# Performance work log

Measured on AMD Instinct MI355X. Metric: run time of the kernel, lower is better.

Reference implementation:

```python
import jax, jax.numpy as jnp
import numpy as np

SR = 22050
FLOOR = 60.0
BPO = 12

def _interp_linear(p, T):
    # torch F.interpolate(mode='linear', align_corners=False)
    S = p.shape[0]
    x = np.clip((np.arange(T, dtype=np.float64) + 0.5) * (S / T) - 0.5, 0.0, S - 1)
    i0 = np.floor(x).astype(np.int64)
    i1 = np.minimum(i0 + 1, S - 1)
    f = (x - i0).astype(np.float32)
    return p[i0] * (1.0 - f) + p[i1] * f

def _hann(n):
    # torch.hann_window(n, periodic=True)
    if n <= 0:
        return np.zeros((0,), np.float32)
    return (0.5 - 0.5 * np.cos(2.0 * np.pi * np.arange(n) / n)).astype(np.float32)

def _find_voiced(f0, i):
    sub = f0[i:]
    if sub.size == 0:
        return None
    flag = (sub > 0.0).astype(np.int64)
    flag[0] = 0
    if not flag.any():
        return None
    rel = int(flag.argmax())
    after = flag[rel:]
    z = np.nonzero(after == 0)[0]
    run = int(z[0]) if z.size else int(after.size)
    return i + rel, i + rel + run

def _l2n(v):
    # F.normalize(dim=-1), eps=1e-12
    return v / np.maximum(np.linalg.norm(v, axis=-1, keepdims=True), 1e-12)

def _find_peak(signal, f0, i, right_dir):
    w = int(SR / max(float(f0[i]), FLOOR))
    s = max(i - w // 2, 0)
    if right_dir:
        cand_l, cand_r = int(i + 0.3 * w), int(i + 0.75 * w)
    else:
        cand_l, cand_r = max(int(i - 1.75 * w), 0), max(int(i - 1.3 * w), 0)
    if cand_l == cand_r or len(signal) - cand_l < w:
        return w, -1.0, i, 0.0
    seg = np.lib.stride_tricks.sliding_window_view(signal[cand_l:cand_r + w], w)
    corr = _l2n(seg) @ _l2n(signal[s:s + w])
    r = int(corr.argmax())
    return w, float(corr[r]), i + (r + cand_l) - s, float(np.abs(seg[r]).max())

def _find_allpeaks(signal, f0):
    gp = float(np.abs(signal).max())
    added_right, i, peaks = -1e308, 0, []
    while True:
        voiced = _find_voiced(f0, i)
        if voiced is None:
            break
        left, right = voiced
        middle = (left + right) // 2
        w = int(SR / float(f0[middle]))
        s = max(middle - w // 2, 0)
        seg = signal[s:s + w]
        mn, imn = float(seg.min()), int(seg.argmin())
        mx, imx = float(seg.max()), int(seg.argmax())
        i = middle if mn == mx else s + (imn if abs(mn) > abs(mx) else imx)
        backup = i
        while True:
            w, corr, i, peak = _find_peak(signal, f0, i, False)
            if corr == -1.0:
                i -= w
            if i < left:
                if corr > 0.7 and peak > 0.023333 * gp and i - added_right > 0.8 * w:
                    peaks.append(i)
                break
            if corr > 0.3 and (peak == 0.0 or peak > 0.01 * gp):
                if i - added_right > 0.8 * w:
                    peaks.append(i)
        i = backup
        while True:
            w, corr, i, peak = _find_peak(signal, f0, i, True)
            if corr == -1.0:
                i += w
            if i >= right:
                if corr > 0.7 and peak > 0.023333 * gp:
                    peaks.append(i)
                    added_right = i
                break
            if corr > 0.3 and (peak == 0.0 or peak > 0.01 * gp):
                peaks.append(i)
                added_right = i
        i = right
    if not peaks:
        return None
    return np.clip(np.array(sorted(peaks), dtype=np.int64), 0, len(signal) - 1)

def _psola_plan(signal, pitch, peaks):
    # Returns list of (dst_idx, src_idx, window) overlap-add ops plus tail index.
    T = len(signal)
    idx = np.arange(T)
    max_w = 1.25 * SR / float(pitch[pitch > 0].min())
    ops, i = [], 0
    while i < T:
        voiced = _find_voiced(pitch, i)
        if voiced is None:
            break
        left_v, right_v = voiced
        if i < left_v:
            ops.append((idx[i:left_v], idx[i:left_v], _hann(left_v - i)))
        while left_v < right_v:
            p = int(np.abs(peaks - left_v).argmin())
            period = int(SR / max(float(pitch[left_v]), FLOOR))
            left_w = right_w = period // 2
            if p > 0 and peaks[p] - peaks[p - 1] <= max_w:
                left_w = min(int(peaks[p] - peaks[p - 1]), left_w)
            if p < len(peaks) - 1 and peaks[p + 1] - peaks[p] <= max_w:
                right_w = min(int(peaks[p + 1] - peaks[p]), right_w)
            left_i = max(int(peaks[p]) - left_w, 0)
            right_i = int(peaks[p]) + right_w
            ival = (right_i - left_i) // 2
            if ival <= 0:  # safety guard; unreachable for speech-range pitch
                break
            win = _hann(ival * 2)
            seglen = min(len(idx[left_v - ival:left_v + ival]), len(idx[left_i:left_i + ival * 2]))
            dst = idx[left_v - ival:left_v - ival + seglen]
            src = idx[left_i:left_i + seglen]
            L = min(len(dst), len(src), seglen)
            ops.append((dst[:L], src[:L], win[:L]))
            left_v += ival * 2
        i = right_v
    return ops, i

def _pitch_shift_plan(snd, pitch, steps, pitch_range):
    if not (pitch > 1e-05).any():
        return None
    f0 = _interp_linear(pitch, len(snd))
    peaks = _find_allpeaks(snd, f0)
    if peaks is None:
        return None
    v = np.sort(pitch[pitch > 0.0])
    median = float(v[(len(v) - 1) // 2])  # torch lower median
    factor = 2.0 ** (steps / BPO)
    f0, median = f0 * factor, median * factor
    f0 = np.where(f0 > 0.0, median + (f0 - median) * pitch_range, 0.0).astype(np.float32)
    return _psola_plan(snd, f0, peaks)

def setup_inputs():
    key = jax.random.key(0)
    T, S = 661500, 3000
    t = np.arange(S)
    base = (170.0 + 40.0 * np.sin(2.0 * np.pi * t / 400.0)).astype(np.float32)
    voiced = (t % 75) >= 15  # alternating unvoiced/voiced runs
    pitch = np.where(voiced, base, 0.0).astype(np.float32)
    f0 = _interp_linear(pitch, T)
    phase = 2.0 * np.pi * np.cumsum(f0.astype(np.float64)) / SR
    noise = np.asarray(jax.random.normal(key, (T,)), np.float32)
    snd = np.where(f0 > 0.0, 0.55 * np.sin(phase) + 0.25 * np.sin(2 * phase) + 0.1 * np.sin(3 * phase), 0.0)
    snd = np.clip(snd + 0.02 * noise, -1.0, 1.0).astype(np.float32)
    return {"snd": jnp.asarray(snd), "pitch": jnp.asarray(pitch), "steps": 3, "pitch_range": jnp.float32(1.0)}

def reference(snd, pitch, steps, pitch_range):
    snd_np = np.asarray(snd, np.float32)
    pitch_np = np.asarray(pitch, np.float32)
    plan = _pitch_shift_plan(snd_np, pitch_np, int(steps), float(pitch_range))
    if plan is None:
        return jnp.asarray(snd_np)
    ops, tail = plan
    out = np.zeros_like(snd_np)
    for dst, src, win in ops:
        out[dst] += win * snd_np[src]
    out[tail:] = snd_np[tail:]
    return jnp.asarray(out)
```

## Files before the change

kernel.cpp:

```cpp
#include <hip/hip_runtime.h>
#include <cfloat>
#include <climits>
#include <math.h>

#define SRATE 22050.0
#define WMAX 512
#define RCAP 128
#define LCR 256
#define RCR 512
#define SCAP 16384
#define OPR 256
#define MSL 3072
#define NTW 256
#define NTM 1024
#define PCAP 8192
#define FCAP 16384
#define PSTG 4096
#define SNDW 15872
#define RPW 136


__global__ __launch_bounds__(256) void kstats(const float* __restrict__ pitch, int S, unsigned* scal) {
  __shared__ float sp[MSL];
  __shared__ int sc[256];
  __shared__ int sa[256];
  __shared__ unsigned hist[256];
  __shared__ unsigned sprefix, smask;
  __shared__ int srank;
  int tid = threadIdx.x;
  if (tid < 64) scal[tid] = (tid == 1) ? 0x7f800000u : 0u;
  bool lds = (S <= MSL);
  int c = 0, a = 0;
  for (int j = tid; j < S; j += 256) {
    float v = pitch[j];
    if (lds) sp[j] = v;
    if (v > 0.0f) c++;
    if (v > 1e-05f) a = 1;
  }
  sc[tid] = c; sa[tid] = a; __syncthreads();
  for (int st = 128; st; st >>= 1) {
    if (tid < st) { sc[tid] += sc[tid + st]; sa[tid] |= sa[tid + st]; }
    __syncthreads();
  }
  int n = sc[0];
  if (tid == 0) { scal[15] = (unsigned)n; scal[3] = (unsigned)sa[0]; }
  if (n == 0) return;
  if (tid == 0) { sprefix = 0u; smask = 0u; srank = (n - 1) >> 1; }
  __syncthreads();
  for (int shift = 24; shift >= 0; shift -= 8) {
    hist[tid] = 0u;
    __syncthreads();
    unsigned pfx = sprefix, msk = smask;
    for (int q = tid; q < S; q += 256) {
      float v = lds ? sp[q] : pitch[q];
      if (v > 0.0f) {
        unsigned u = __float_as_uint(v);
        if ((u & msk) == pfx) atomicAdd(&hist[(u >> shift) & 255u], 1u);
      }
    }
    __syncthreads();
    if (tid == 0) {
      int r = srank;
      unsigned b = 0;
      for (;;) { unsigned cc = hist[b]; if (r < (int)cc) break; r -= (int)cc; b++; }
      srank = r;
      sprefix = pfx | (b << shift);
      smask = msk | (0xFFu << shift);
    }
    __syncthreads();
  }
  if (tid == 0) scal[2] = sprefix;
}

__device__ __forceinline__ float interp1(const float* __restrict__ pitch, int S, double r, int t) {
  double x = ((double)t + 0.5) * r - 0.5;
  if (x < 0.0) x = 0.0;
  double sm1 = (double)(S - 1);
  if (x > sm1) x = sm1;
  double fl = floor(x);
  int i0 = (int)fl;
  int i1 = i0 + 1; if (i1 > S - 1) i1 = S - 1;
  float f = (float)(x - fl);
  return __fadd_rn(__fmul_rn(pitch[i0], __fsub_rn(1.0f, f)), __fmul_rn(pitch[i1], f));
}

__global__ __launch_bounds__(256) void kprep(const float* __restrict__ pitch, int S, int T,
                                             const float* __restrict__ snd, unsigned* scal,
                                             const int* __restrict__ steps_p, const float* __restrict__ pr_p,
                                             float* __restrict__ f0, float* __restrict__ f0s,
                                             int* __restrict__ pd, int* __restrict__ w0,
                                             int* s0l, int* e0l, int* s1l, int* e1l) {
  __shared__ float smax[256];
  __shared__ unsigned smin[256];
  float med = __uint_as_float(scal[2]);
  double factor = exp2((double)steps_p[0] / 12.0);
  float fac32 = (float)factor;
  float m32 = (float)((double)med * factor);
  float pr32 = pr_p[0];
  double r = (double)S / (double)T;
  float amax = 0.0f;
  unsigned lmin = 0x7f800000u;
  int stride = gridDim.x * blockDim.x;
  for (int t = blockIdx.x * blockDim.x + threadIdx.x; t < T; t += stride) {
    float v = interp1(pitch, S, r, t);
    f0[t] = v;
    float v1 = __fmul_rn(v, fac32);
    float vs = 0.0f;
    if (v1 > 0.0f) vs = __fadd_rn(m32, __fmul_rn(__fsub_rn(v1, m32), pr32));
    f0s[t] = vs;
    { double fd = (double)vs; if (fd < 60.0) fd = 60.0; pd[t] = (int)(SRATE / fd); }
    { double fi = (double)v; if (fi < 60.0) fi = 60.0;
      int ww = (int)(SRATE / fi); if (ww < 1) ww = 1; if (ww > WMAX - 1) ww = WMAX - 1;
      w0[t] = ww; }
    if (vs > 0.0f) { unsigned b = __float_as_uint(vs); if (b < lmin) lmin = b; }
    float a = fabsf(snd[t]); if (a > amax) amax = a;
    bool pv = false, pv1 = false;
    if (t > 0) {
      float pvv = interp1(pitch, S, r, t - 1);
      pv = pvv > 0.0f;
      float pm1 = __fmul_rn(pvv, fac32);
      float pvs = 0.0f;
      if (pm1 > 0.0f) pvs = __fadd_rn(m32, __fmul_rn(__fsub_rn(pm1, m32), pr32));
      pv1 = pvs > 0.0f;
    }
    bool cv = v > 0.0f, cv1 = vs > 0.0f;
    if (cv && (t == 0 || !pv))  { unsigned k = atomicAdd(scal + 8, 1u);  if (k < RCAP) s0l[k] = t; }
    if (!cv && t > 0 && pv)     { unsigned k = atomicAdd(scal + 9, 1u);  if (k < RCAP) e0l[k] = t; }
    if (cv1 && (t == 0 || !pv1)){ unsigned k = atomicAdd(scal + 10, 1u); if (k < RCAP) s1l[k] = t; }
    if (!cv1 && t > 0 && pv1)   { unsigned k = atomicAdd(scal + 11, 1u); if (k < RCAP) e1l[k] = t; }
  }
  smax[threadIdx.x] = amax; smin[threadIdx.x] = lmin; __syncthreads();
  for (int st = 128; st; st >>= 1) {
    if (threadIdx.x < st) {
      float o = smax[threadIdx.x + st]; if (o > smax[threadIdx.x]) smax[threadIdx.x] = o;
      unsigned u = smin[threadIdx.x + st]; if (u < smin[threadIdx.x]) smin[threadIdx.x] = u;
    }
    __syncthreads();
  }
  if (threadIdx.x == 0) {
    atomicMax(scal + 0, __float_as_uint(smax[0]));
    atomicMin(scal + 1, smin[0]);
  }
}

__device__ void ranksort(int* a, int n, int tid, int* tmp) {
  int v = 0, rk = 0;
  if (tid < n) {
    v = a[tid];
    for (int q = 0; q < n; q++) if (a[q] < v) rk++;
  }
  __syncthreads();
  if (tid < n) tmp[rk] = v;
  __syncthreads();
  if (tid < n) a[tid] = tmp[tid];
  __syncthreads();
}

__device__ int pair_regions_lds(float f1, int T, int* sl, int ns, int* el, int ne, int* L, int* R) {
  int b = 0;
  if (ns > 0 && sl[0] == 0) {
    if (T > 1 && f1 > 0.0f) sl[0] = 1;
    else b = 1;
  }
  int m = 0, j = 0;
  for (int k = b; k < ns; k++) {
    int Lv = sl[k];
    while (j < ne && el[j] <= Lv) j++;
    int Rv = (j < ne) ? el[j] : T;
    if (m < RCAP) { L[m] = Lv; R[m] = Rv; m++; }
  }
  return m;
}

__global__ __launch_bounds__(128) void kregsort2(const float* __restrict__ f0, const float* __restrict__ f0s,
                                                 int T, unsigned* scal,
                                                 const int* __restrict__ s0l, const int* __restrict__ e0l,
                                                 const int* __restrict__ s1l, const int* __restrict__ e1l,
                                                 int* r0L, int* r0R, int* r1L, int* r1R) {
  __shared__ int A[RCAP], B[RCAP], C[RCAP], D[RCAP];
  __shared__ int tmp[RCAP];
  __shared__ int LA[RCAP], RA[RCAP];
  int tid = threadIdx.x;
  int ns0 = min((int)scal[8], RCAP), ne0 = min((int)scal[9], RCAP);
  int ns1 = min((int)scal[10], RCAP), ne1 = min((int)scal[11], RCAP);
  if (tid < ns0) A[tid] = s0l[tid];
  if (tid < ne0) B[tid] = e0l[tid];
  if (tid < ns1) C[tid] = s1l[tid];
  if (tid < ne1) D[tid] = e1l[tid];
  __syncthreads();
  ranksort(A, ns0, tid, tmp);
  ranksort(B, ne0, tid, tmp);
  ranksort(C, ns1, tid, tmp);
  ranksort(D, ne1, tid, tmp);
  float f0_1 = (T > 1) ? f0[1] : 0.0f;
  float f0s_1 = (T > 1) ? f0s[1] : 0.0f;
  __shared__ int m0s, m1s;
  if (tid == 0) {
    m0s = pair_regions_lds(f0_1, T, A, ns0, B, ne0, LA, RA);
  }
  __syncthreads();
  if (tid < m0s) { r0L[tid] = LA[tid]; r0R[tid] = RA[tid]; }
  __syncthreads();
  if (tid == 0) {
    m1s = pair_regions_lds(f0s_1, T, C, ns1, D, ne1, LA, RA);
  }
  __syncthreads();
  if (tid < m1s) { r1L[tid] = LA[tid]; r1R[tid] = RA[tid]; }
  if (tid == 0) { scal[12] = (unsigned)m0s; scal[13] = (unsigned)m1s; }
}

struct FPRes { int w; int i; float corr; float peak; };
struct FPG { int w, s, cl, nw, rlen; bool ok; };

__device__ __forceinline__ FPG fp_geom(int T, int i, int w, bool right_dir) {
  FPG g;
  int s = i - w / 2; if (s < 0) s = 0;
  int cl, cr;
  if (right_dir) {
    cl = (int)((double)i + 0.3 * (double)w);
    cr = (int)((double)i + 0.75 * (double)w);
  } else {
    double al = (double)i - 1.75 * (double)w;
    double bl = (double)i - 1.3 * (double)w;
    cl = (int)al; if (cl < 0) cl = 0;
    cr = (int)bl; if (cr < 0) cr = 0;
  }
  g.w = w; g.s = s; g.cl = cl;
  g.ok = !(cl == cr || T - cl < w);
  int nw = (((cr + w) < T ? (cr + w) : T)) - cl - w + 1;
  if (nw < 1) nw = 1;
  g.nw = nw;
  int rlen = T - s; if (rlen > w) rlen = w;
  g.rlen = rlen;
  return g;
}

template <bool L>
__device__ __forceinline__ FPRes fp_impl(const float* __restrict__ snd, const float* lsnd, int wb0,
                                         FPG g, int i, int tid,
                                         float (*refp)[RPW], double* sdd, float* swf, int* swi, float* swp) {
  FPRes res;
  int w = g.w, s = g.s, cl = g.cl, nw = g.nw, rlen = g.rlen;
  res.w = w;
  int lane = tid & 63, wv = tid >> 6;
  double part = 0.0;
  for (int k = tid; k < w; k += NTW) {
    float v = (k < rlen) ? (L ? lsnd[s + k - wb0] : snd[s + k]) : 0.0f;
    refp[k & 3][k >> 2] = v;
    part += (double)v * (double)v;
  }
  for (int off = 32; off; off >>= 1) part += __shfl_xor(part, off, 64);
  if (lane == 0) sdd[wv] = part;
  __syncthreads();
  double refden = sqrt(sdd[0] + sdd[1] + sdd[2] + sdd[3]);
  if (refden < 1e-12) refden = 1e-12;
  int gg = tid >> 2, sub = tid & 3;
  float bestv = -FLT_MAX; int bestr = INT_MAX; float bestp = 0.0f;
  for (int base = 0; base < nw; base += 64) {
    int r = base + gg;
    if (r < nw) {
      const float* seg = (L ? (lsnd + (cl - wb0)) : (snd + cl)) + r;
      const float* rrow = refp[sub];
      double d0 = 0.0, d1 = 0.0, n0 = 0.0, n1 = 0.0;
      float pkc = 0.0f;
      int k = sub, j = 0;
      for (; k + 12 < w; k += 16, j += 4) {
        float4 rv = *reinterpret_cast<const float4*>(rrow + j);
        float a0f = seg[k], a1f = seg[k + 4];
        pkc = fmaxf(pkc, fabsf(a0f));
        pkc = fmaxf(pkc, fabsf(a1f));
        double a0 = (double)a0f, a1 = (double)a1f;
        d0 += a0 * (double)rv.x; n0 += a0 * a0;
        d1 += a1 * (double)rv.y; n1 += a1 * a1;
        float a2f = seg[k + 8], a3f = seg[k + 12];
        pkc = fmaxf(pkc, fabsf(a2f));
        pkc = fmaxf(pkc, fabsf(a3f));
        double a2 = (double)a2f, a3 = (double)a3f;
        d0 += a2 * (double)rv.z; n0 += a2 * a2;
        d1 += a3 * (double)rv.w; n1 += a3 * a3;
      }
      for (; k + 4 < w; k += 8) {
        float a0f = seg[k], a1f = seg[k + 4];
        pkc = fmaxf(pkc, fabsf(a0f));
        pkc = fmaxf(pkc, fabsf(a1f));
        double a0 = (double)a0f, b0 = (double)refp[k & 3][k >> 2];
        double a1 = (double)a1f, b1 = (double)refp[(k + 4) & 3][(k + 4) >> 2];
        d0 += a0 * b0; n0 += a0 * a0;
        d1 += a1 * b1; n1 += a1 * a1;
      }
      for (; k < w; k += 4) {
        float af = seg[k];
        pkc = fmaxf(pkc, fabsf(af));
        double a = (double)af; d0 += a * (double)refp[k & 3][k >> 2]; n0 += a * a;
      }
      double dot = d0 + d1, nr2 = n0 + n1;
      dot += __shfl_xor(dot, 1, 64); nr2 += __shfl_xor(nr2, 1, 64);
      pkc = fmaxf(pkc, __shfl_xor(pkc, 1, 64));
      dot += __shfl_xor(dot, 2, 64); nr2 += __shfl_xor(nr2, 2, 64);
      pkc = fmaxf(pkc, __shfl_xor(pkc, 2, 64));
      if (sub == 0) {
        double den = sqrt(nr2); if (den < 1e-12) den = 1e-12;
        float c = (float)(dot / (den * refden));
        if (c > bestv) { bestv = c; bestr = r; bestp = pkc; }
      }
    }
  }
  for (int off = 32; off >= 4; off >>= 1) {
    float ov = __shfl_xor(bestv, off, 64);
    int orr = __shfl_xor(bestr, off, 64);
    float op = __shfl_xor(bestp, off, 64);
    if (ov > bestv || (ov == bestv && orr < bestr)) { bestv = ov; bestr = orr; bestp = op; }
  }
  if (lane == 0) { swf[wv] = bestv; swi[wv] = bestr; swp[wv] = bestp; }
  __syncthreads();
  float bv = swf[0]; int br = swi[0]; float bp = swp[0];
  for (int q = 1; q < 4; q++) {
    float ov = swf[q]; int orr = swi[q]; float op = swp[q];
    if (ov > bv || (ov == bv && orr < br)) { bv = ov; br = orr; bp = op; }
  }
  res.corr = bv;
  res.i = i + (br + cl) - s;
  res.peak = bp;
  return res;
}

__device__ __forceinline__ FPRes find_peak_block(const float* __restrict__ snd,
                                                 const float* lsnd, int wb0, int wb1, bool useW,
                                                 int T, int i, int wcur, bool right_dir, int tid,
                                                 float (*refp)[RPW], double* sdd,
                                                 float* swf, int* swi, float* swp) {
  FPG g = fp_geom(T, i, wcur, right_dir);
  if (!g.ok) { FPRes r; r.w = g.w; r.corr = -1.0f; r.i = i; r.peak = 0.0f; return r; }
  int lo_a = g.s < g.cl ? g.s : g.cl;
  int hi1 = g.s + g.w, hi2 = g.cl + g.nw + g.w;
  int hi_a = hi1 > hi2 ? hi1 : hi2;
  bool inW = useW && lo_a >= wb0 && hi_a <= wb1;
  if (inW) return fp_impl<true>(snd, lsnd, wb0, g, i, tid, refp, sdd, swf, swi, swp);
  return fp_impl<false>(snd, lsnd, wb0, g, i, tid, refp, sdd, swf, swi, swp);
}

__global__ __launch_bounds__(NTW) void kwalk(const float* __restrict__ snd,
                                             const float* __restrict__ pitch, int S,
                                             const int* __restrict__ w0,
                                             int T, const unsigned* scal,
                                             const int* __restrict__ r0L, const int* __restrict__ r0R,
                                             int2* __restrict__ lcand, int* __restrict__ lcnt,
                                             int* __restrict__ rpk, int* __restrict__ rcnt) {
  __shared__ float lsnd[SNDW];
  __shared__ short swtab[SNDW];
  __shared__ __align__(16) float refp[4][RPW];
  __shared__ double sdd[4];
  __shared__ float swf[8];
  __shared__ int swi[8];
  __shared__ float swp[4];
  __shared__ float spitch[PSTG];
  int tid = threadIdx.x;
  int lane = tid & 63, wv = tid >> 6;
  if (scal[3] == 0u) return;
  bool useL = (S <= PSTG);
  if (useL) { for (int k = tid; k < S; k += NTW) spitch[k] = pitch[k]; }
  __syncthreads();
  double rr = (double)S / (double)T;
  int nreg = (int)scal[12];
  float gp = __uint_as_float(scal[0]);
  for (int wid = blockIdx.x; wid < 2 * nreg; wid += gridDim.x) {
    int r = wid >> 1;
    bool rightdir = (wid & 1) != 0;
    int left = r0L[r], right = r0R[r];
    int middle = (left + right) >> 1;
    int wb0 = left - 1024; if (wb0 < 0) wb0 = 0;
    int wb1 = right + 1024; if (wb1 > T) wb1 = T;
    bool useW = (wb1 - wb0) <= SNDW;
    __syncthreads();
    if (useW) {
      for (int k = tid; k < wb1 - wb0; k += NTW) {
        lsnd[k] = snd[wb0 + k];
        swtab[k] = (short)w0[wb0 + k];
      }
    }
    __syncthreads();
    double fm = useL ? (double)interp1(spitch, S, rr, middle) : (double)interp1(pitch, S, rr, middle);
    double wd = SRATE / fm;
    long long wcap = 2LL * (long long)T;
    int w = (wd >= (double)wcap) ? (int)wcap : (int)wd;
    if (w < 1) w = 1;
    int s0 = middle - w / 2; if (s0 < 0) s0 = 0;
    int wlen = w; if (wlen > T - s0) wlen = T - s0;
    float lmn = FLT_MAX; int lmni = INT_MAX;
    float lmx = -FLT_MAX; int lmxi = INT_MAX;
    for (int k = tid; k < wlen; k += NTW) {
      int idx = s0 + k;
      float v = (useW && idx >= wb0 && idx < wb1) ? lsnd[idx - wb0] : snd[idx];
      if (v < lmn) { lmn = v; lmni = k; }
      if (v > lmx) { lmx = v; lmxi = k; }
    }
    for (int off = 32; off; off >>= 1) {
      float ov = __shfl_xor(lmn, off, 64); int oi = __shfl_xor(lmni, off, 64);
      if (ov < lmn || (ov == lmn && oi < lmni)) { lmn = ov; lmni = oi; }
      float ov2 = __shfl_xor(lmx, off, 64); int oi2 = __shfl_xor(lmxi, off, 64);
      if (ov2 > lmx || (ov2 == lmx && oi2 < lmxi)) { lmx = ov2; lmxi = oi2; }
    }
    if (lane == 0) { swf[wv] = lmn; swi[wv] = lmni; swf[4 + wv] = lmx; swi[4 + wv] = lmxi; }
    __syncthreads();
    float mn = swf[0]; int imn = swi[0];
    float mx = swf[4]; int imx = swi[4];
    for (int q = 1; q < 4; q++) {
      float ov = swf[q]; int oi = swi[q];
      if (ov < mn || (ov == mn && oi < imn)) { mn = ov; imn = oi; }
      float ov2 = swf[4 + q]; int oi2 = swi[4 + q];
      if (ov2 > mx || (ov2 == mx && oi2 < imx)) { mx = ov2; imx = oi2; }
    }
    __syncthreads();
    int i;
    if (mn == mx) i = middle;
    else i = s0 + ((fabsf(mn) > fabsf(mx)) ? imn : imx);
    if (!rightdir) {
      int nl = 0, guard = 0;
      for (;;) {
        if (++guard > 500000) break;
        int wcur;
        if (useW && i >= wb0 && i < wb1) wcur = (int)swtab[i - wb0];
        else {
          double fi = useL ? (double)interp1(spitch, S, rr, i) : (double)interp1(pitch, S, rr, i);
          if (fi < 60.0) fi = 60.0;
          int ww = (int)(SRATE / fi); if (ww < 1) ww = 1; if (ww > WMAX - 1) ww = WMAX - 1;
          wcur = ww;
        }
        FPRes p = find_peak_block(snd, lsnd, wb0, wb1, useW, T, i, wcur, false, tid,
                                  refp, sdd, swf, swi, swp);
        i = p.i;
        if (p.corr == -1.0f) i -= p.w;
        if (i < left) {
          if ((double)p.corr > 0.7 && (double)p.peak > 0.023333 * (double)gp) {
            if (nl < LCR) { if (tid == 0) lcand[r * LCR + nl] = make_int2(i, p.w); nl++; }
          }
          break;
        }
        if ((double)p.corr > 0.3 && (p.peak == 0.0f || (double)p.peak > 0.01 * (double)gp)) {
          if (nl < LCR) { if (tid == 0) lcand[r * LCR + nl] = make_int2(i, p.w); nl++; }
        }
      }
      if (tid == 0) lcnt[r] = nl;
    } else {
      int nr = 0, guard = 0;
      for (;;) {
        if (++guard > 500000) break;
        int wcur;
        if (useW && i >= wb0 && i < wb1) wcur = (int)swtab[i - wb0];
        else {
          double fi = useL ? (double)interp1(spitch, S, rr, i) : (double)interp1(pitch, S, rr, i);
          if (fi < 60.0) fi = 60.0;
          int ww = (int)(SRATE / fi); if (ww < 1) ww = 1; if (ww > WMAX - 1) ww = WMAX - 1;
          wcur = ww;
        }
        FPRes p = find_peak_block(snd, lsnd, wb0, wb1, useW, T, i, wcur, true, tid,
                                  refp, sdd, swf, swi, swp);
        i = p.i;
        if (p.corr == -1.0f) i += p.w;
        if (i >= right) {
          if ((double)p.corr > 0.7 && (double)p.peak > 0.023333 * (double)gp) {
            if (nr < RCR) { if (tid == 0) rpk[r * RCR + nr] = i; nr++; }
          }
          break;
        }
        if ((double)p.corr > 0.3 && (p.peak == 0.0f || (double)p.peak > 0.01 * (double)gp)) {
          if (nr < RCR) { if (tid == 0) rpk[r * RCR + nr] = i; nr++; }
        }
      }
      if (tid == 0) rcnt[r] = nr;
    }
  }
}

__global__ __launch_bounds__(NTM) void kmerge(int T, unsigned* scal,
                                              const int2* __restrict__ lcand, const int* __restrict__ lcnt,
                                              const int* __restrict__ rpk, const int* __restrict__ rcnt,
                                              int* __restrict__ peaks) {
  __shared__ long long arR[RCAP];
  __shared__ long long lastR[RCAP];
  __shared__ int rcs[RCAP];
  __shared__ int lcs[RCAP];
  __shared__ int klc[RCAP];
  __shared__ int off[RCAP + 1];
  __shared__ int sbuf[SCAP];
  __shared__ int unsorted;
  int tid = threadIdx.x;
  int lane = tid & 63, wv = tid >> 6;
  int nreg = (int)scal[12];
  if (scal[3] == 0u || nreg == 0) { if (tid == 0) scal[4] = 0u; return; }
  if (tid < nreg) {
    int rc = rcnt[tid];
    rcs[tid] = rc;
    lcs[tid] = lcnt[tid];
    lastR[tid] = (rc > 0) ? (long long)rpk[tid * RCR + rc - 1] : LLONG_MIN;
  }
  __syncthreads();
  if (tid == 0) {
    long long ar = -(1LL << 62);
    for (int r = 0; r < nreg; r++) { arR[r] = ar; if (rcs[r] > 0) ar = lastR[r]; }
  }
  __syncthreads();
  for (int r = wv; r < nreg; r += 16) {
    int n = lcs[r];
    long long ar = arR[r];
    int cnt = 0;
    for (int base = 0; base < n; base += 64) {
      int jp = base + lane;
      bool pred = false;
      if (jp < n) {
        int j = n - 1 - jp;
        int2 cd = lcand[r * LCR + j];
        pred = ((double)((long long)cd.x - ar) > 0.8 * (double)cd.y);
      }
      unsigned long long m = __ballot(pred);
      cnt += __popcll(m);
    }
    if (lane == 0) klc[r] = cnt;
  }
  __syncthreads();
  if (tid == 0) {
    int acc = 0;
    for (int r = 0; r < nreg; r++) { off[r] = acc; acc += klc[r] + rcs[r]; if (acc > SCAP) acc = SCAP; }
    off[nreg] = acc;
    scal[4] = (unsigned)acc;
    unsorted = 0;
  }
  __syncthreads();
  for (int r = wv; r < nreg; r += 16) {
    long long ar = arR[r];
    int n = lcs[r];
    int pos0 = off[r];
    for (int base = 0; base < n; base += 64) {
      int jp = base + lane;
      bool pred = false; int val = 0;
      if (jp < n) {
        int j = n - 1 - jp;
        int2 cd = lcand[r * LCR + j];
        if ((double)((long long)cd.x - ar) > 0.8 * (double)cd.y) { pred = true; val = cd.x; }
      }
      unsigned long long m = __ballot(pred);
      if (pred) {
        int pre = __popcll(m & ((1ull << lane) - 1ull));
        int pos = pos0 + pre;
        if (pos < SCAP) peaks[pos] = val;
      }
      pos0 += __popcll(m);
    }
    int rc = rcs[r];
    for (int j = lane; j < rc; j += 64) {
      int pos = pos0 + j;
      if (pos < SCAP) peaks[pos] = rpk[r * RCR + j];
    }
  }
  __syncthreads();
  int npk = off[nreg];
  if (npk > 1) {
    for (int k = tid; k < npk - 1; k += NTM) {
      if (peaks[k] > peaks[k + 1]) unsorted = 1;
    }
    __syncthreads();
    if (unsorted) {
      int n2 = 1; while (n2 < npk) n2 <<= 1;
      for (int k = tid; k < n2; k += NTM) sbuf[k] = (k < npk) ? peaks[k] : INT_MAX;
      __syncthreads();
      for (int kk = 2; kk <= n2; kk <<= 1) {
        for (int j = kk >> 1; j > 0; j >>= 1) {
          for (int idx = tid; idx < n2; idx += NTM) {
            int ixj = idx ^ j;
            if (ixj > idx) {
              int a = sbuf[idx], b = sbuf[ixj];
              bool up = ((idx & kk) == 0);
              if ((up && a > b) || (!up && a < b)) { sbuf[idx] = b; sbuf[ixj] = a; }
            }
          }
          __syncthreads();
        }
      }
      for (int k = tid; k < npk; k += NTM) peaks[k] = sbuf[k];
      __syncthreads();
    }
  }
  for (int k = tid; k < npk; k += NTM) { int v = peaks[k]; if (v < 0) v = 0; if (v > T - 1) v = T - 1; peaks[k] = v; }
}

__global__ __launch_bounds__(256) void kplan(const int* __restrict__ pd, int T, unsigned* scal,
                                             const int* __restrict__ peaks,
                                             const int* __restrict__ r1L, const int* __restrict__ r1R,
                                             int4* __restrict__ ops, int* __restrict__ opcnt) {
  __shared__ int sp[PCAP];
  __shared__ int ib[FCAP];
  int tid = threadIdx.x;
  int npk = (int)scal[4];
  int nreg = (int)scal[13];
  int r = (int)blockIdx.x;
  if (scal[3] == 0u || npk == 0) {
    if (r == 0 && tid == 0) { scal[6] = 0u; scal[14] = 0u; }
    return;
  }
  if (r == 0 && tid == 0) {
    scal[6] = (nreg > 0) ? (unsigned)r1R[nreg - 1] : 0u;
    scal[14] = (unsigned)nreg;
  }
  if (r >= nreg) return;
  int prev_right = (r == 0) ? 0 : r1R[r - 1];
  int left_v = r1L[r], right_v = r1R[r];
  int pl_n = npk < PCAP ? npk : PCAP;
  int pl4 = pl_n & ~3;
  for (int k = tid * 4; k < pl4; k += 1024) {
    int4 v = *reinterpret_cast<const int4*>(peaks + k);
    sp[k] = v.x; sp[k + 1] = v.y; sp[k + 2] = v.z; sp[k + 3] = v.w;
  }
  for (int k = pl4 + tid; k < pl_n; k += 256) sp[k] = peaks[k];
  int span = right_v - left_v;
  int fl_n = span < FCAP ? span : FCAP;
  const int* srcp = pd + left_v;
  int head = (4 - (left_v & 3)) & 3; if (head > fl_n) head = fl_n;
  for (int k = tid; k < head; k += 256) ib[k] = srcp[k];
  int rem4 = (fl_n - head) & ~3;
  for (int k = tid * 4; k < rem4; k += 1024) {
    int4 v = *reinterpret_cast<const int4*>(srcp + head + k);
    ib[head + k] = v.x; ib[head + k + 1] = v.y; ib[head + k + 2] = v.z; ib[head + k + 3] = v.w;
  }
  for (int k = head + rem4 + tid; k < fl_n; k += 256) ib[k] = srcp[k];
  __syncthreads();
  if (tid != 0) return;

  auto PRD = [&](int idx) -> int { return (idx < pl_n) ? sp[idx] : peaks[idx]; };

  double minpos = (double)__uint_as_float(scal[1]);
  double max_w = 1.25 * SRATE / minpos;
  int c = 0;
  if (prev_right < left_v) {
    ops[r * OPR + c] = make_int4(prev_right, prev_right, left_v - prev_right, left_v - prev_right);
    c++;
  }
  int lv = left_v, guard = 0;
  int lo = -1;
  int Pm2 = 0, Pm1 = 0, P0 = 0, P1 = 0;
  while (lv < right_v) {
    if (++guard > 500000) break;
    int fo = lv - left_v;
    int period = (fo < fl_n) ? ib[fo] : pd[lv];
    int x = lv;
    if (lo < 0) {
      int a = 0, b = npk;
      while (a < b) { int m = (a + b) >> 1; if (PRD(m) < x) a = m + 1; else b = m; }
      lo = a;
      Pm2 = (lo - 2 >= 0) ? PRD(lo - 2) : 0;
      Pm1 = (lo - 1 >= 0) ? PRD(lo - 1) : 0;
      P0  = (lo < npk) ? PRD(lo) : 0;
      P1  = (lo + 1 < npk) ? PRD(lo + 1) : 0;
    } else {
      while (lo < npk && P0 < x) {
        lo++;
        Pm2 = Pm1; Pm1 = P0; P0 = P1;
        P1 = (lo + 1 < npk) ? PRD(lo + 1) : 0;
      }
    }
    long long d0 = (lo > 0) ? (long long)x - (long long)Pm1 : LLONG_MAX;
    long long d1 = (lo < npk) ? (long long)P0 - (long long)x : LLONG_MAX;
    int p, Pp, Ppm1, Pp1;
    if (d0 <= d1) {
      p = lo - 1;
      int tv = Pm1;
      if (p > 0 && Pm2 == tv) {
        while (p > 0 && PRD(p - 1) == tv) p--;
        Pp = tv;
        Ppm1 = (p > 0) ? PRD(p - 1) : 0;
        Pp1 = (p < npk - 1) ? PRD(p + 1) : 0;
      } else {
        Pp = Pm1; Ppm1 = Pm2; Pp1 = P0;
      }
    } else {
      p = lo; Pp = P0; Ppm1 = Pm1; Pp1 = P1;
    }
    int lw = period >> 1, rw = period >> 1;
    if (p > 0) { long long gp_ = (long long)Pp - (long long)Ppm1; if ((double)gp_ <= max_w && gp_ < (long long)lw) lw = (int)gp_; }
    if (p < npk - 1) { long long gp_ = (long long)Pp1 - (long long)Pp; if ((double)gp_ <= max_w && gp_ < (long long)rw) rw = (int)gp_; }
    int left_i = Pp - lw; if (left_i < 0) left_i = 0;
    int right_i = Pp + rw;
    int ival = (right_i - left_i) >> 1;
    if (ival <= 0) break;
    int a0 = lv - ival;
    int len1 = 0;
    if (a0 >= 0) { int e = lv + ival; if (e > T) e = T; len1 = e - a0; if (len1 < 0) len1 = 0; }
    int e2 = left_i + 2 * ival; if (e2 > T) e2 = T;
    int len2 = e2 - left_i; if (len2 < 0) len2 = 0;
    int seglen = len1 < len2 ? len1 : len2;
    int len_dst = (a0 < 0) ? 0 : ((T - a0 < seglen) ? T - a0 : seglen);
    int len_src = (T - left_i < seglen) ? T - left_i : seglen;
    int L = seglen; if (len_dst < L) L = len_dst; if (len_src < L) L = len_src;
    if (L > 0 && c < OPR) { ops[r * OPR + c] = make_int4(a0, left_i, L, 2 * ival); c++; }
    lv += 2 * ival;
  }
  opcnt[r] = c;
}

__global__ __launch_bounds__(256) void kapply(const float* __restrict__ snd, float* __restrict__ out,
                                              const unsigned* scal, const int4* __restrict__ ops,
                                              const int* __restrict__ opcnt) {
  int nreg = (int)scal[14];
  int total = nreg * OPR;
  for (int slot = blockIdx.x; slot < total; slot += gridDim.x) {
    int r = slot / OPR, j = slot - r * OPR;
    if (j >= opcnt[r]) continue;
    int4 o = ops[r * OPR + j];
    double nn = (double)o.w;
    for (int k = threadIdx.x; k < o.z; k += blockDim.x) {
      double cph = (6.283185307179586 * (double)k) / nn;
      float wv = (float)(0.5 - 0.5 * cos(cph));
      atomicAdd(out + o.x + k, __fmul_rn(wv, snd[o.y + k]));
    }
  }
}

__global__ __launch_bounds__(256) void ktail(const float* __restrict__ snd, float* __restrict__ out,
                                             const unsigned* scal, int T) {
  int tail = (int)scal[6];
  int stride = gridDim.x * blockDim.x;
  for (int t = blockIdx.x * blockDim.x + threadIdx.x; t < T; t += stride)
    if (t >= tail) out[t] = snd[t];
}

extern "C" void kernel_launch(void* const* d_in, const int* in_sizes, int n_in,
                              void* d_out, int out_size, void* d_ws, size_t ws_size,
                              hipStream_t stream) {
  (void)n_in; (void)ws_size;
  int T = in_sizes[0];
  int S = in_sizes[1];
  const float* snd = (const float*)d_in[0];
  const float* pitch = (const float*)d_in[1];
  const int* steps = (const int*)d_in[2];
  const float* prange = (const float*)d_in[3];
  float* out = (float*)d_out;

  char* base = (char*)d_ws;
  size_t off = 0;
  auto alloc = [&](size_t bytes, size_t align) -> char* {
    off = (off + align - 1) & ~(align - 1);
    char* p = base + off;
    off += bytes;
    return p;
  };
  float* f0  = (float*)alloc((size_t)T * 4, 16);
  float* f0s = (float*)alloc((size_t)T * 4, 16);
  int* pd    = (int*)alloc((size_t)T * 4, 16);
  int* w0    = (int*)alloc((size_t)T * 4, 16);
  unsigned* scal = (unsigned*)alloc(256, 16);
  int* s0l = (int*)alloc(RCAP * 4, 4);
  int* e0l = (int*)alloc(RCAP * 4, 4);
  int* s1l = (int*)alloc(RCAP * 4, 4);
  int* e1l = (int*)alloc(RCAP * 4, 4);
  int* r0L = (int*)alloc(RCAP * 4, 4);
  int* r0R = (int*)alloc(RCAP * 4, 4);
  int* r1L = (int*)alloc(RCAP * 4, 4);
  int* r1R = (int*)alloc(RCAP * 4, 4);
  int* lcnt = (int*)alloc(RCAP * 4, 4);
  int* rcnt = (int*)alloc(RCAP * 4, 4);
  int* opcnt = (int*)alloc(RCAP * 4, 4);
  int2* lcand = (int2*)alloc((size_t)RCAP * LCR * 8, 8);
  int* rpk = (int*)alloc((size_t)RCAP * RCR * 4, 4);
  int* peaks = (int*)alloc((size_t)SCAP * 4, 16);
  int4* ops = (int4*)alloc((size_t)RCAP * OPR * 16, 16);

  hipMemsetAsync(d_out, 0, (size_t)out_size * sizeof(float), stream);
  kstats<<<1, 256, 0, stream>>>(pitch, S, scal);
  kprep<<<1024, 256, 0, stream>>>(pitch, S, T, snd, scal, steps, prange, f0, f0s, pd, w0, s0l, e0l, s1l, e1l);
  kregsort2<<<1, 128, 0, stream>>>(f0, f0s, T, scal, s0l, e0l, s1l, e1l, r0L, r0R, r1L, r1R);
  kwalk<<<256, NTW, 0, stream>>>(snd, pitch, S, w0, T, scal, r0L, r0R, lcand, lcnt, rpk, rcnt);
  kmerge<<<1, NTM, 0, stream>>>(T, scal, lcand, lcnt, rpk, rcnt, peaks);
  kplan<<<RCAP, 256, 0, stream>>>(pd, T, scal, peaks, r1L, r1R, ops, opcnt);
  kapply<<<2048, 256, 0, stream>>>(snd, out, scal, ops, opcnt);
  ktail<<<1024, 256, 0, stream>>>(snd, out, scal, T);
}
```

Baseline: 462.4 us.

## Fuse apply and tail kernels, drop f0 buffers, reuse neighbor interp via shuffle

Merges the overlap-add apply kernel and the tail-copy kernel into one launch, with separate block ranges, and clips apply writes at the tail boundary so the two ranges never write the same element. Removes the full-length f0/f0s global arrays, since only element 1 was ever read; that value is now stashed in scal. The t-1 interpolation is replaced by a wave shuffle except at lane 0. Together these save one launch, two full-length global writes, and redundant interpolation work. The tail clip relies on the tail copy overwriting those positions anyway, which matches the reference assignment out[tail:] = snd[tail:].

```diff
diff --git a/kernel.cpp b/kernel.cpp
--- a/kernel.cpp
+++ b/kernel.cpp
@@ -18,6 +18,8 @@
 #define PSTG 4096
 #define SNDW 15872
 #define RPW 136
+#define APPLYB 2048
+#define TAILB 1024
 
 
 __global__ __launch_bounds__(256) void kstats(const float* __restrict__ pitch, int S, unsigned* scal) {
@@ -87,7 +89,6 @@
 __global__ __launch_bounds__(256) void kprep(const float* __restrict__ pitch, int S, int T,
                                              const float* __restrict__ snd, unsigned* scal,
                                              const int* __restrict__ steps_p, const float* __restrict__ pr_p,
-                                             float* __restrict__ f0, float* __restrict__ f0s,
                                              int* __restrict__ pd, int* __restrict__ w0,
                                              int* s0l, int* e0l, int* s1l, int* e1l) {
   __shared__ float smax[256];
@@ -100,14 +101,14 @@
   double r = (double)S / (double)T;
   float amax = 0.0f;
   unsigned lmin = 0x7f800000u;
+  int lane = threadIdx.x & 63;
   int stride = gridDim.x * blockDim.x;
   for (int t = blockIdx.x * blockDim.x + threadIdx.x; t < T; t += stride) {
     float v = interp1(pitch, S, r, t);
-    f0[t] = v;
     float v1 = __fmul_rn(v, fac32);
     float vs = 0.0f;
     if (v1 > 0.0f) vs = __fadd_rn(m32, __fmul_rn(__fsub_rn(v1, m32), pr32));
-    f0s[t] = vs;
+    if (t == 1) { scal[16] = __float_as_uint(v); scal[17] = __float_as_uint(vs); }
     { double fd = (double)vs; if (fd < 60.0) fd = 60.0; pd[t] = (int)(SRATE / fd); }
     { double fi = (double)v; if (fi < 60.0) fi = 60.0;
       int ww = (int)(SRATE / fi); if (ww < 1) ww = 1; if (ww > WMAX - 1) ww = WMAX - 1;
@@ -115,8 +116,9 @@
     if (vs > 0.0f) { unsigned b = __float_as_uint(vs); if (b < lmin) lmin = b; }
     float a = fabsf(snd[t]); if (a > amax) amax = a;
     bool pv = false, pv1 = false;
+    float upv = __shfl_up(v, 1, 64);
     if (t > 0) {
-      float pvv = interp1(pitch, S, r, t - 1);
+      float pvv = (lane == 0) ? interp1(pitch, S, r, t - 1) : upv;
       pv = pvv > 0.0f;
       float pm1 = __fmul_rn(pvv, fac32);
       float pvs = 0.0f;
@@ -172,8 +174,7 @@
   return m;
 }
 
-__global__ __launch_bounds__(128) void kregsort2(const float* __restrict__ f0, const float* __restrict__ f0s,
-                                                 int T, unsigned* scal,
+__global__ __launch_bounds__(128) void kregsort2(int T, unsigned* scal,
                                                  const int* __restrict__ s0l, const int* __restrict__ e0l,
                                                  const int* __restrict__ s1l, const int* __restrict__ e1l,
                                                  int* r0L, int* r0R, int* r1L, int* r1R) {
@@ -192,8 +193,8 @@
   ranksort(B, ne0, tid, tmp);
   ranksort(C, ns1, tid, tmp);
   ranksort(D, ne1, tid, tmp);
-  float f0_1 = (T > 1) ? f0[1] : 0.0f;
-  float f0s_1 = (T > 1) ? f0s[1] : 0.0f;
+  float f0_1 = (T > 1) ? __uint_as_float(scal[16]) : 0.0f;
+  float f0s_1 = (T > 1) ? __uint_as_float(scal[17]) : 0.0f;
   __shared__ int m0s, m1s;
   if (tid == 0) {
     m0s = pair_regions_lds(f0_1, T, A, ns0, B, ne0, LA, RA);
@@ -696,30 +697,32 @@
   opcnt[r] = c;
 }
 
-__global__ __launch_bounds__(256) void kapply(const float* __restrict__ snd, float* __restrict__ out,
-                                              const unsigned* scal, const int4* __restrict__ ops,
-                                              const int* __restrict__ opcnt) {
-  int nreg = (int)scal[14];
-  int total = nreg * OPR;
-  for (int slot = blockIdx.x; slot < total; slot += gridDim.x) {
-    int r = slot / OPR, j = slot - r * OPR;
-    if (j >= opcnt[r]) continue;
-    int4 o = ops[r * OPR + j];
-    double nn = (double)o.w;
-    for (int k = threadIdx.x; k < o.z; k += blockDim.x) {
-      double cph = (6.283185307179586 * (double)k) / nn;
-      float wv = (float)(0.5 - 0.5 * cos(cph));
-      atomicAdd(out + o.x + k, __fmul_rn(wv, snd[o.y + k]));
-    }
-  }
-}
-
-__global__ __launch_bounds__(256) void ktail(const float* __restrict__ snd, float* __restrict__ out,
-                                             const unsigned* scal, int T) {
+__global__ __launch_bounds__(256) void kout(const float* __restrict__ snd, float* __restrict__ out,
+                                            const unsigned* scal, const int4* __restrict__ ops,
+                                            const int* __restrict__ opcnt, int T) {
   int tail = (int)scal[6];
-  int stride = gridDim.x * blockDim.x;
-  for (int t = blockIdx.x * blockDim.x + threadIdx.x; t < T; t += stride)
-    if (t >= tail) out[t] = snd[t];
+  if (blockIdx.x < APPLYB) {
+    int nreg = (int)scal[14];
+    int total = nreg * OPR;
+    for (int slot = blockIdx.x; slot < total; slot += APPLYB) {
+      int r = slot / OPR, j = slot - r * OPR;
+      if (j >= opcnt[r]) continue;
+      int4 o = ops[r * OPR + j];
+      double nn = (double)o.w;
+      int kend = o.z;
+      { int lim = tail - o.x; if (lim < 0) lim = 0; if (kend > lim) kend = lim; }
+      for (int k = threadIdx.x; k < kend; k += blockDim.x) {
+        double cph = (6.283185307179586 * (double)k) / nn;
+        float wv = (float)(0.5 - 0.5 * cos(cph));
+        atomicAdd(out + o.x + k, __fmul_rn(wv, snd[o.y + k]));
+      }
+    }
+  } else {
+    int b = blockIdx.x - APPLYB;
+    int stride = TAILB * 256;
+    for (int t = b * 256 + threadIdx.x; t < T; t += stride)
+      if (t >= tail) out[t] = snd[t];
+  }
 }
 
 extern "C" void kernel_launch(void* const* d_in, const int* in_sizes, int n_in,
@@ -742,8 +745,6 @@
     off += bytes;
     return p;
   };
-  float* f0  = (float*)alloc((size_t)T * 4, 16);
-  float* f0s = (float*)alloc((size_t)T * 4, 16);
   int* pd    = (int*)alloc((size_t)T * 4, 16);
   int* w0    = (int*)alloc((size_t)T * 4, 16);
   unsigned* scal = (unsigned*)alloc(256, 16);
@@ -765,11 +766,10 @@
 
   hipMemsetAsync(d_out, 0, (size_t)out_size * sizeof(float), stream);
   kstats<<<1, 256, 0, stream>>>(pitch, S, scal);
-  kprep<<<1024, 256, 0, stream>>>(pitch, S, T, snd, scal, steps, prange, f0, f0s, pd, w0, s0l, e0l, s1l, e1l);
-  kregsort2<<<1, 128, 0, stream>>>(f0, f0s, T, scal, s0l, e0l, s1l, e1l, r0L, r0R, r1L, r1R);
+  kprep<<<1024, 256, 0, stream>>>(pitch, S, T, snd, scal, steps, prange, pd, w0, s0l, e0l, s1l, e1l);
+  kregsort2<<<1, 128, 0, stream>>>(T, scal, s0l, e0l, s1l, e1l, r0L, r0R, r1L, r1R);
   kwalk<<<256, NTW, 0, stream>>>(snd, pitch, S, w0, T, scal, r0L, r0R, lcand, lcnt, rpk, rcnt);
   kmerge<<<1, NTM, 0, stream>>>(T, scal, lcand, lcnt, rpk, rcnt, peaks);
   kplan<<<RCAP, 256, 0, stream>>>(pd, T, scal, peaks, r1L, r1R, ops, opcnt);
-  kapply<<<2048, 256, 0, stream>>>(snd, out, scal, ops, opcnt);
-  ktail<<<1024, 256, 0, stream>>>(snd, out, scal, T);
-}
+  kout<<<APPLYB + TAILB, 256, 0, stream>>>(snd, out, scal, ops, opcnt, T);
+}
```

Measured after the change: 458.2 us (median of 2 runs). Within noise of the previous version (-0.9%).
